# Kernel tuning notes

Measured on AMD Instinct MI355X. Metric: run time of the kernel, lower is better.

The kernel has to match this reference:

```python
import jax, jax.numpy as jnp
import numpy as np

N_NODES = 100_000
N_EDGES = 4_000_000


def setup_inputs() -> dict:
    key = jax.random.key(0)
    k1, k2, k3, k4 = jax.random.split(key, 4)
    frac_coords = jax.random.uniform(k1, (N_NODES, 3), dtype=jnp.float32)
    edge_indices = jax.random.randint(k2, (2, N_EDGES), 0, N_NODES, dtype=jnp.int32)
    symmops = jax.random.normal(k3, (N_EDGES, 4, 4), dtype=jnp.float32)
    cell_translations = jax.random.normal(k4, (N_EDGES, 3), dtype=jnp.float32)
    return {
        "frac_coords": frac_coords,
        "edge_indices": edge_indices,
        "symmops": symmops,
        "cell_translations": cell_translations,
    }


def reference(frac_coords, edge_indices, symmops, cell_translations):
    # Gather node positions for each edge (NodePosition with selection_index [0, 1]).
    in_frac = frac_coords[edge_indices[0]]   # (M, 3)
    out_frac = frac_coords[edge_indices[1]]  # (M, 3)
    # Homogeneous coordinate: (M, 4)
    out_h = jnp.concatenate([out_frac, jnp.ones_like(out_frac[:, :1])], axis=1)
    # Per-edge 4x4 affine transform, keep first 3 components.
    out_t = jnp.einsum('ij,ikj->ik', out_h, symmops)[:, :3]
    # Periodic wrap into [0, 1) then shift by cell translation.
    out_t = out_t - jnp.floor(out_t) + cell_translations
    # Displacement vector per edge.
    return in_frac - out_t
```

## Files before the change

kernel.cpp:

```cpp
#include <hip/hip_runtime.h>


__global__ __launch_bounds__(256) void disp_vec_kernel(
    const float* __restrict__ frac,
    const int*   __restrict__ eidx,
    const float* __restrict__ symm,
    const float* __restrict__ ct,
    float*       __restrict__ out,
    int M)
{
    int i = blockIdx.x * blockDim.x + threadIdx.x;
    if (i >= M) return;

    int n0 = eidx[i];
    int n1 = eidx[M + i];

    const float* f0 = frac + (size_t)n0 * 3;
    const float* f1 = frac + (size_t)n1 * 3;
    float in_x = f0[0], in_y = f0[1], in_z = f0[2];
    float ox   = f1[0], oy   = f1[1], oz   = f1[2];

    const float4* s = (const float4*)(symm + (size_t)i * 16);
    float4 r0 = s[0];
    float4 r1 = s[1];
    float4 r2 = s[2];

    float t0 = ox * r0.x + oy * r0.y + oz * r0.z + r0.w;
    float t1 = ox * r1.x + oy * r1.y + oz * r1.z + r1.w;
    float t2 = ox * r2.x + oy * r2.y + oz * r2.z + r2.w;

    t0 -= floorf(t0);
    t1 -= floorf(t1);
    t2 -= floorf(t2);

    const float* c = ct + (size_t)i * 3;
    t0 += c[0];
    t1 += c[1];
    t2 += c[2];

    float* o = out + (size_t)i * 3;
    o[0] = in_x - t0;
    o[1] = in_y - t1;
    o[2] = in_z - t2;
}

extern "C" void kernel_launch(void* const* d_in, const int* in_sizes, int n_in,
                              void* d_out, int out_size, void* d_ws, size_t ws_size,
                              hipStream_t stream) {
    const float* frac = (const float*)d_in[0];
    const int*   eidx = (const int*)d_in[1];
    const float* symm = (const float*)d_in[2];
    const float* ct   = (const float*)d_in[3];
    float* out = (float*)d_out;

    const int M = in_sizes[1] / 2;

    const int block = 256;
    const int grid = (M + block - 1) / block;
    disp_vec_kernel<<<grid, block, 0, stream>>>(frac, eidx, symm, ct, out, M);
}
```

Baseline: 429.2 us.

## Pad node coords to float4, stage translations/output via LDS, nontemporal loads

Adds a pre-pass that packs the node coordinates into a 16-byte-aligned float4 workspace so each edge gathers its two nodes with single vector loads. The main kernel stages the cell translations and the outputs through shared memory so global reads and writes are coalesced 16-byte accesses. Streaming inputs use nontemporal loads and stores. In exchange it adds an extra kernel launch, several block barriers, and a scalar tail kernel for leftover edges.

```diff
diff --git a/kernel.cpp b/kernel.cpp
--- a/kernel.cpp
+++ b/kernel.cpp
@@ -1,15 +1,90 @@
 #include <hip/hip_runtime.h>
 
 
-__global__ __launch_bounds__(256) void disp_vec_kernel(
-    const float* __restrict__ frac,
+typedef float vf4 __attribute__((ext_vector_type(4)));
+
+__global__ __launch_bounds__(256) void pad_frac_kernel(
+    const float* __restrict__ frac, vf4* __restrict__ fracp, int N)
+{
+    int i = blockIdx.x * blockDim.x + threadIdx.x;
+    if (i < N) {
+        vf4 v;
+        v.x = frac[3 * i + 0];
+        v.y = frac[3 * i + 1];
+        v.z = frac[3 * i + 2];
+        v.w = 0.0f;
+        fracp[i] = v;
+    }
+}
+
+__global__ __launch_bounds__(256) void disp_vec_main(
+    const vf4*   __restrict__ fracp,
     const int*   __restrict__ eidx,
     const float* __restrict__ symm,
     const float* __restrict__ ct,
     float*       __restrict__ out,
     int M)
 {
-    int i = blockIdx.x * blockDim.x + threadIdx.x;
+    __shared__ float lds[768];
+    const int tid  = threadIdx.x;
+    const int base = blockIdx.x * 256;
+    const int i    = base + tid;
+
+    if (tid < 192) {
+        const vf4* c4 = (const vf4*)(ct + (size_t)base * 3);
+        ((vf4*)lds)[tid] = __builtin_nontemporal_load(c4 + tid);
+    }
+
+    const int n0 = __builtin_nontemporal_load(eidx + i);
+    const int n1 = __builtin_nontemporal_load(eidx + M + i);
+
+    const vf4* s = (const vf4*)(symm + (size_t)i * 16);
+    const vf4 r0 = __builtin_nontemporal_load(s + 0);
+    const vf4 r1 = __builtin_nontemporal_load(s + 1);
+    const vf4 r2 = __builtin_nontemporal_load(s + 2);
+
+    const vf4 fin = fracp[n0];
+    const vf4 fo  = fracp[n1];
+
+    float t0 = fo.x * r0.x + fo.y * r0.y + fo.z * r0.z + r0.w;
+    float t1 = fo.x * r1.x + fo.y * r1.y + fo.z * r1.z + r1.w;
+    float t2 = fo.x * r2.x + fo.y * r2.y + fo.z * r2.z + r2.w;
+
+    t0 -= floorf(t0);
+    t1 -= floorf(t1);
+    t2 -= floorf(t2);
+
+    __syncthreads();
+    const float c0 = lds[3 * tid + 0];
+    const float c1 = lds[3 * tid + 1];
+    const float c2 = lds[3 * tid + 2];
+
+    const float o0 = fin.x - (t0 + c0);
+    const float o1 = fin.y - (t1 + c1);
+    const float o2 = fin.z - (t2 + c2);
+
+    __syncthreads();
+    lds[3 * tid + 0] = o0;
+    lds[3 * tid + 1] = o1;
+    lds[3 * tid + 2] = o2;
+    __syncthreads();
+
+    if (tid < 192) {
+        vf4* o4 = (vf4*)(out + (size_t)base * 3);
+        __builtin_nontemporal_store(((vf4*)lds)[tid], o4 + tid);
+    }
+    (void)M;
+}
+
+__global__ __launch_bounds__(256) void disp_vec_scalar(
+    const float* __restrict__ frac,
+    const int*   __restrict__ eidx,
+    const float* __restrict__ symm,
+    const float* __restrict__ ct,
+    float*       __restrict__ out,
+    int M, int start)
+{
+    int i = start + blockIdx.x * blockDim.x + threadIdx.x;
     if (i >= M) return;
 
     int n0 = eidx[i];
@@ -17,14 +92,11 @@
 
     const float* f0 = frac + (size_t)n0 * 3;
     const float* f1 = frac + (size_t)n1 * 3;
-    float in_x = f0[0], in_y = f0[1], in_z = f0[2];
-    float ox   = f1[0], oy   = f1[1], oz   = f1[2];
 
     const float4* s = (const float4*)(symm + (size_t)i * 16);
-    float4 r0 = s[0];
-    float4 r1 = s[1];
-    float4 r2 = s[2];
+    float4 r0 = s[0], r1 = s[1], r2 = s[2];
 
+    float ox = f1[0], oy = f1[1], oz = f1[2];
     float t0 = ox * r0.x + oy * r0.y + oz * r0.z + r0.w;
     float t1 = ox * r1.x + oy * r1.y + oz * r1.z + r1.w;
     float t2 = ox * r2.x + oy * r2.y + oz * r2.z + r2.w;
@@ -34,14 +106,10 @@
     t2 -= floorf(t2);
 
     const float* c = ct + (size_t)i * 3;
-    t0 += c[0];
-    t1 += c[1];
-    t2 += c[2];
-
     float* o = out + (size_t)i * 3;
-    o[0] = in_x - t0;
-    o[1] = in_y - t1;
-    o[2] = in_z - t2;
+    o[0] = f0[0] - (t0 + c[0]);
+    o[1] = f0[1] - (t1 + c[1]);
+    o[2] = f0[2] - (t2 + c[2]);
 }
 
 extern "C" void kernel_launch(void* const* d_in, const int* in_sizes, int n_in,
@@ -53,9 +121,23 @@
     const float* ct   = (const float*)d_in[3];
     float* out = (float*)d_out;
 
+    const int N = in_sizes[0] / 3;
     const int M = in_sizes[1] / 2;
 
-    const int block = 256;
-    const int grid = (M + block - 1) / block;
-    disp_vec_kernel<<<grid, block, 0, stream>>>(frac, eidx, symm, ct, out, M);
+    const size_t need = (size_t)N * sizeof(vf4);
+    if (ws_size >= need) {
+        vf4* fracp = (vf4*)d_ws;
+        pad_frac_kernel<<<(N + 255) / 256, 256, 0, stream>>>(frac, fracp, N);
+
+        const int full_tiles = M / 256;
+        const int rem        = M % 256;
+        if (full_tiles > 0) {
+            disp_vec_main<<<full_tiles, 256, 0, stream>>>(fracp, eidx, symm, ct, out, M);
+        }
+        if (rem > 0) {
+            disp_vec_scalar<<<1, 256, 0, stream>>>(frac, eidx, symm, ct, out, M, full_tiles * 256);
+        }
+    } else {
+        disp_vec_scalar<<<(M + 255) / 256, 256, 0, stream>>>(frac, eidx, symm, ct, out, M, 0);
+    }
 }
```

Result: no change. 433.9 us (+1.1%).
